# Performance work log

Hardware: AMD Instinct MI355X
Metric: run time of the kernel (lower is better)

## Reference

```python
import jax, jax.numpy as jnp
import numpy as np

N = 20000      # nodes
E = 400000     # directed edges
F_IN = 256     # node features
H, C = 16, 32  # heads, per-head channels (out_channels + beta_on, beta_on=0)
OUT = 32       # out_channels
HID = 128      # 4 * out_channels


def setup_inputs() -> dict:
    key = jax.random.key(0)
    ks = jax.random.split(key, 14)
    s = 0.05
    return {
        "x": jax.random.normal(ks[0], (N, F_IN), jnp.float32),
        "edge_index": jax.random.randint(ks[1], (2, E), 0, N, jnp.int32),
        "W1": jax.random.normal(ks[2], (F_IN, H * C), jnp.float32) * s,
        "att_src1": jax.random.normal(ks[3], (H, C), jnp.float32) * s,
        "att_dst1": jax.random.normal(ks[4], (H, C), jnp.float32) * s,
        "b1": jax.random.normal(ks[5], (C,), jnp.float32) * s,
        "W2": jax.random.normal(ks[6], (F_IN, H * C), jnp.float32) * s,
        "att_src2": jax.random.normal(ks[7], (H, C), jnp.float32) * s,
        "att_dst2": jax.random.normal(ks[8], (H, C), jnp.float32) * s,
        "b2": jax.random.normal(ks[9], (C,), jnp.float32) * s,
        "lin1_w": jax.random.normal(ks[10], (F_IN, HID), jnp.float32) * s,
        "lin1_b": jax.random.normal(ks[11], (HID,), jnp.float32) * s,
        "lin2_w": jax.random.normal(ks[12], (HID, OUT), jnp.float32) * s,
        "lin2_b": jax.random.normal(ks[13], (OUT,), jnp.float32) * s,
    }


def gat_conv(x, W, att_src, att_dst, bias, src, dst):
    """PyG GATConv: heads=H, concat=False (mean over heads), no self loops.
    src = message source node per edge, dst = aggregation (central) node."""
    h = (x @ W).reshape(-1, H, C)                 # [N, H, C]
    a_s = jnp.sum(h * att_src, axis=-1)           # [N, H]
    a_d = jnp.sum(h * att_dst, axis=-1)           # [N, H]
    alpha = jax.nn.leaky_relu(a_s[src] + a_d[dst], 0.2)  # [E, H]
    # numerically-stable segment softmax over edges grouped by dst
    m = jax.lax.stop_gradient(jax.ops.segment_max(alpha, dst, num_segments=N))
    m = jnp.where(jnp.isfinite(m), m, 0.0)        # empty segments -> -inf
    ex = jnp.exp(alpha - m[dst])                  # [E, H]
    den = jax.ops.segment_sum(ex, dst, num_segments=N)   # [N, H]
    coef = ex / (den[dst] + 1e-16)                # [E, H]
    msg = h[src] * coef[:, :, None]               # [E, H, C]
    out = jax.ops.segment_sum(msg, dst, num_segments=N)  # [N, H, C]
    return out.mean(axis=1) + bias                # concat=False -> head mean


def reference(x, edge_index, W1, att_src1, att_dst1, b1, W2, att_src2, att_dst2,
              b2, lin1_w, lin1_b, lin2_w, lin2_b):
    src = edge_index[0]
    dst = edge_index[1]
    # conv1: flow='source_to_target' -> aggregate at edge_index[1]
    x_in = jax.nn.elu(gat_conv(x, W1, att_src1, att_dst1, b1, src, dst))
    # conv2: flow='target_to_source' -> aggregate at edge_index[0]
    x_out = jax.nn.elu(gat_conv(x, W2, att_src2, att_dst2, b2, dst, src))
    x1 = jax.nn.elu(x @ lin1_w + lin1_b)
    x_self = jax.nn.elu(x1 @ lin2_w + lin2_b)
    return (x_in, x_out, x_self)
```

## Files before the change

### kernel.cpp

```cpp
#include <hip/hip_runtime.h>
#include <math.h>

#define NN 20000
#define EE 400000
#define FIN 256
#define HH 16
#define CC 32
#define HC 512
#define H8W 1024
#define HIDN 128
#define OUTC 32
#define WT 1024

typedef unsigned short u16;
typedef unsigned char u8;
typedef __attribute__((ext_vector_type(8))) short short8v;
typedef __attribute__((ext_vector_type(4))) float f32x4;
typedef __attribute__((ext_vector_type(2))) float f32x2;

__device__ inline u16 f2bf(float f) {
  unsigned u = __builtin_bit_cast(unsigned, f);
  unsigned r = (u + 0x7fffu + ((u >> 16) & 1u)) >> 16;
  return (u16)r;
}
__device__ inline float bf2f(u16 b) {
  unsigned u = ((unsigned)b) << 16;
  return __builtin_bit_cast(float, u);
}

__device__ __forceinline__ void gload16(const u16* g, u16* l) {
  __builtin_amdgcn_global_load_lds(
      (const __attribute__((address_space(1))) unsigned int*)g,
      (__attribute__((address_space(3))) unsigned int*)l, 16, 0, 0);
}

__device__ __forceinline__ void fp8x8_fma2(uint2 hv, float w, f32x2* acc) {
  f32x2 w2; w2.x = w; w2.y = w;
  f32x2 p0 = __builtin_amdgcn_cvt_pk_f32_fp8(hv.x, false);
  f32x2 p1 = __builtin_amdgcn_cvt_pk_f32_fp8(hv.x, true);
  f32x2 p2 = __builtin_amdgcn_cvt_pk_f32_fp8(hv.y, false);
  f32x2 p3 = __builtin_amdgcn_cvt_pk_f32_fp8(hv.y, true);
  acc[0] += p0 * w2;
  acc[1] += p1 * w2;
  acc[2] += p2 * w2;
  acc[3] += p3 * w2;
}

__global__ void k_prep_hist(const float* __restrict__ x, u16* __restrict__ xb,
                            const float* __restrict__ W1, const float* __restrict__ W2,
                            u16* __restrict__ wtc,
                            const float* __restrict__ L1, u16* __restrict__ lt1,
                            const float* __restrict__ L2, u16* __restrict__ lt2,
                            const int* __restrict__ ei, int* __restrict__ cur) {
  int b = blockIdx.x, t = threadIdx.x;
  if (b < 2500) {
    int i = b * 256 + t;
    float4 v0 = ((const float4*)x)[i * 2];
    float4 v1 = ((const float4*)x)[i * 2 + 1];
    short8v o;
    o[0] = (short)f2bf(v0.x); o[1] = (short)f2bf(v0.y);
    o[2] = (short)f2bf(v0.z); o[3] = (short)f2bf(v0.w);
    o[4] = (short)f2bf(v1.x); o[5] = (short)f2bf(v1.y);
    o[6] = (short)f2bf(v1.z); o[7] = (short)f2bf(v1.w);
    *(short8v*)(xb + (size_t)i * 8) = o;
  } else if (b < 3524) {
    int i = (b - 2500) * 256 + t;
    int n = i >> 8, k = i & 255;
    wtc[i] = f2bf(n < 512 ? W1[k * HC + n] : W2[k * HC + (n - 512)]);
  } else if (b < 3652) {
    int i = (b - 3524) * 256 + t;
    int n = i >> 8, k = i & 255;
    lt1[i] = f2bf(L1[k * HIDN + n]);
  } else if (b < 3668) {
    int i = (b - 3652) * 256 + t;
    int n = i >> 7, k = i & 127;
    lt2[i] = f2bf(L2[k * OUTC + n]);
  } else {
    int e = (b - 3668) * 256 + t;
    if (e < EE) {
      atomicAdd(&cur[ei[EE + e]], 1);
      atomicAdd(&cur[NN + ei[e]], 1);
    }
  }
}

__device__ void scan_one(int* cur, int* off, int* part) {
  const int t = threadIdx.x;
  const int CHK = 20;
  int base = t * CHK;
  int loc[CHK];
  int s = 0;
#pragma unroll
  for (int i = 0; i < CHK; ++i) {
    int idx = base + i;
    int v = (idx < NN) ? cur[idx] : 0;
    loc[i] = s;
    s += v;
  }
  part[t] = s;
  __syncthreads();
  for (int d = 1; d < 1024; d <<= 1) {
    int v2 = (t >= d) ? part[t - d] : 0;
    __syncthreads();
    part[t] += v2;
    __syncthreads();
  }
  int cbase = part[t] - s;
#pragma unroll
  for (int i = 0; i < CHK; ++i) {
    int idx = base + i;
    if (idx < NN) {
      int o = cbase + loc[i];
      off[idx] = o;
      cur[idx] = o;
    }
  }
  if (t == 1023) off[NN] = part[1023];
}

__global__ __launch_bounds__(1024) void k_scan(int* cur, int* off1, int* off2) {
  __shared__ int part[1024];
  if (blockIdx.x == 0) scan_one(cur, off1, part);
  else                 scan_one(cur + NN, off2, part);
}

__global__ void k_scatter(const int* __restrict__ ei, int* cur,
                          int* __restrict__ adj1, int* __restrict__ adj2) {
  int e = blockIdx.x * 256 + threadIdx.x;
  if (e < EE) {
    int s1 = ei[e], d1 = ei[EE + e];
    int p1 = atomicAdd(&cur[d1], 1);
    adj1[p1] = s1;
    int p2 = atomicAdd(&cur[NN + s1], 1);
    adj2[p2] = d1;
  }
}

__global__ __launch_bounds__(256) void k_gemm_big(const u16* __restrict__ A,
                                                  const u16* __restrict__ Bt,
                                                  const float* __restrict__ as1,
                                                  const float* __restrict__ ad1,
                                                  const float* __restrict__ as2,
                                                  const float* __restrict__ ad2,
                                                  u8* __restrict__ h8,
                                                  float* __restrict__ a_sA,
                                                  float* __restrict__ a_dA) {
  __shared__ u16 As[128 * 64];
  __shared__ u16 Bs[128 * 64];
  const int hw = blockIdx.x;
  const int logical = (hw & 7) * 157 + (hw >> 3);
  const int bm = (logical >> 3) * 128, bn = logical & 7;
  const int t = threadIdx.x;
  const int lane = t & 63, wave = t >> 6;
  const int wr = (wave >> 1) * 64, wc = (wave & 1) * 64;
  const int l15 = lane & 15, l4 = lane >> 4;
  const int rloc = lane >> 3;
  const int kc_src = (lane & 7) ^ rloc;
  const int K = FIN;

  f32x4 acc[4][4] = {};
  for (int k0 = 0; k0 < K; k0 += 64) {
    __syncthreads();
#pragma unroll
    for (int q = 0; q < 4; ++q) {
      const int rblk = q * 4 + wave;
      const int r = rblk * 8 + rloc;
      gload16(A + (size_t)(bm + r) * K + k0 + kc_src * 8, As + rblk * 512);
      gload16(Bt + (size_t)(bn * 128 + r) * K + k0 + kc_src * 8, Bs + rblk * 512);
    }
    __syncthreads();
#pragma unroll
    for (int kh = 0; kh < 2; ++kh) {
      const int kc = kh * 4 + l4;
      short8v af[4], bfr[4];
#pragma unroll
      for (int i = 0; i < 4; ++i) {
        int row = wr + i * 16 + l15;
        af[i] = *(const short8v*)(As + row * 64 + (kc ^ (row & 7)) * 8);
      }
#pragma unroll
      for (int j = 0; j < 4; ++j) {
        int row = wc + j * 16 + l15;
        bfr[j] = *(const short8v*)(Bs + row * 64 + (kc ^ (row & 7)) * 8);
      }
#pragma unroll
      for (int i = 0; i < 4; ++i)
#pragma unroll
        for (int j = 0; j < 4; ++j)
          acc[i][j] = __builtin_amdgcn_mfma_f32_16x16x32_bf16(af[i], bfr[j], acc[i][j], 0, 0, 0);
    }
  }

  const int conv = bn >> 2;
#pragma unroll
  for (int i = 0; i < 4; ++i)
#pragma unroll
    for (int j = 0; j < 4; ++j)
#pragma unroll
      for (int r = 0; r < 4; ++r) {
        int row = bm + wr + i * 16 + l4 * 4 + r;
        if (row >= NN) continue;
        int colb = bn * 128 + wc + j * 16 + l15;
        float v = acc[i][j][r];
        unsigned e8 = __builtin_amdgcn_cvt_pk_fp8_f32(v, v, 0, false);
        h8[(size_t)row * H8W + colb] = (u8)e8;
      }

  float asv[4], adv[4];
#pragma unroll
  for (int j = 0; j < 4; ++j) {
    int lc = (bn & 3) * 128 + wc + j * 16 + l15;
    int hh = lc >> 5, c = lc & 31;
    asv[j] = (conv ? as2 : as1)[hh * CC + c];
    adv[j] = (conv ? ad2 : ad1)[hh * CC + c];
  }
  const int hA = (bn & 3) * 4 + (wc >> 5);
  float* aS = a_sA + (size_t)conv * NN * HH;
  float* aD = a_dA + (size_t)conv * NN * HH;
#pragma unroll
  for (int i = 0; i < 4; ++i)
#pragma unroll
    for (int r = 0; r < 4; ++r) {
      float sAs = acc[i][0][r] * asv[0] + acc[i][1][r] * asv[1];
      float sAd = acc[i][0][r] * adv[0] + acc[i][1][r] * adv[1];
      float sBs = acc[i][2][r] * asv[2] + acc[i][3][r] * asv[3];
      float sBd = acc[i][2][r] * adv[2] + acc[i][3][r] * adv[3];
#pragma unroll
      for (int m = 1; m < 16; m <<= 1) {
        sAs += __shfl_xor(sAs, m);
        sAd += __shfl_xor(sAd, m);
        sBs += __shfl_xor(sBs, m);
        sBd += __shfl_xor(sBd, m);
      }
      int row = bm + wr + i * 16 + l4 * 4 + r;
      if (l15 == 0 && row < NN) {
        *(float2*)(aS + (size_t)row * HH + hA) = make_float2(sAs, sBs);
        *(float2*)(aD + (size_t)row * HH + hA) = make_float2(sAd, sBd);
      }
    }
}

__global__ __launch_bounds__(256) void k_self(const u16* __restrict__ A,
                                              const u16* __restrict__ lt1,
                                              const u16* __restrict__ lt2,
                                              const float* __restrict__ lin1_b,
                                              const float* __restrict__ lin2_b,
                                              float* __restrict__ outp) {
  __shared__ u16 smem[128 * 128];
  u16* As = smem;
  u16* Bs = smem + 128 * 64;
  const int t = threadIdx.x;
  const int lane = t & 63, wave = t >> 6;
  const int wr = (wave >> 1) * 64, wc = (wave & 1) * 64;
  const int bm = blockIdx.x * 128;
  const int l15 = lane & 15, l4 = lane >> 4;
  const int rloc = lane >> 3;
  const int kc_src = (lane & 7) ^ rloc;
  const int K = FIN;

  f32x4 acc[4][4] = {};
  for (int k0 = 0; k0 < K; k0 += 64) {
    __syncthreads();
#pragma unroll
    for (int q = 0; q < 4; ++q) {
      const int rblk = q * 4 + wave;
      const int r = rblk * 8 + rloc;
      gload16(A + (size_t)(bm + r) * K + k0 + kc_src * 8, As + rblk * 512);
      gload16(lt1 + (size_t)r * K + k0 + kc_src * 8, Bs + rblk * 512);
    }
    __syncthreads();
#pragma unroll
    for (int kh = 0; kh < 2; ++kh) {
      const int kc = kh * 4 + l4;
      short8v af[4], bfr[4];
#pragma unroll
      for (int i = 0; i < 4; ++i) {
        int row = wr + i * 16 + l15;
        af[i] = *(const short8v*)(As + row * 64 + (kc ^ (row & 7)) * 8);
      }
#pragma unroll
      for (int j = 0; j < 4; ++j) {
        int row = wc + j * 16 + l15;
        bfr[j] = *(const short8v*)(Bs + row * 64 + (kc ^ (row & 7)) * 8);
      }
#pragma unroll
      for (int i = 0; i < 4; ++i)
#pragma unroll
        for (int j = 0; j < 4; ++j)
          acc[i][j] = __builtin_amdgcn_mfma_f32_16x16x32_bf16(af[i], bfr[j], acc[i][j], 0, 0, 0);
    }
  }
  __syncthreads();
#pragma unroll
  for (int i = 0; i < 4; ++i)
#pragma unroll
    for (int j = 0; j < 4; ++j)
#pragma unroll
      for (int r = 0; r < 4; ++r) {
        int row = wr + i * 16 + l4 * 4 + r;
        int col = wc + j * 16 + l15;
        float v = acc[i][j][r] + lin1_b[col];
        v = v > 0.f ? v : (expf(v) - 1.f);
        smem[row * 128 + ((((col >> 3) ^ (row & 7))) << 3) + (col & 7)] = f2bf(v);
      }
  __syncthreads();
  f32x4 acc2[2][2] = {};
#pragma unroll
  for (int kk = 0; kk < 4; ++kk) {
    short8v af[2], bfr[2];
#pragma unroll
    for (int i = 0; i < 2; ++i) {
      int row2 = wave * 32 + i * 16 + l15;
      af[i] = *(const short8v*)(smem + row2 * 128 + (((kk * 4 + l4) ^ (row2 & 7)) << 3));
    }
#pragma unroll
    for (int j = 0; j < 2; ++j)
      bfr[j] = *(const short8v*)(lt2 + (size_t)(j * 16 + l15) * 128 + kk * 32 + l4 * 8);
#pragma unroll
    for (int i = 0; i < 2; ++i)
#pragma unroll
      for (int j = 0; j < 2; ++j)
        acc2[i][j] = __builtin_amdgcn_mfma_f32_16x16x32_bf16(af[i], bfr[j], acc2[i][j], 0, 0, 0);
  }
#pragma unroll
  for (int i = 0; i < 2; ++i)
#pragma unroll
    for (int j = 0; j < 2; ++j)
#pragma unroll
      for (int r = 0; r < 4; ++r) {
        int row = bm + wave * 32 + i * 16 + l4 * 4 + r;
        int col = j * 16 + l15;
        if (row < NN) {
          float v = acc2[i][j][r] + lin2_b[col];
          v = v > 0.f ? v : (expf(v) - 1.f);
          outp[(size_t)row * OUTC + col] = v;
        }
      }
}

__global__ __launch_bounds__(256) void k_edge(const int* __restrict__ adj1,
                                              const int* __restrict__ off1,
                                              const int* __restrict__ adj2,
                                              const int* __restrict__ off2,
                                              const float* __restrict__ a_sA,
                                              const float* __restrict__ a_dA,
                                              const u8* __restrict__ h8,
                                              const float* __restrict__ b1,
                                              const float* __restrict__ b2,
                                              float* __restrict__ out) {
  const int wv = threadIdx.x >> 6, lane = threadIdx.x & 63;
  const int gid = blockIdx.x * 4 + wv;
  const int conv = gid >= NN;
  const int node = gid - conv * NN;
  const int* __restrict__ adj = conv ? adj2 : adj1;
  const int* __restrict__ off = conv ? off2 : off1;
  const float* __restrict__ a_s = a_sA + (size_t)conv * NN * HH;
  const float* __restrict__ a_d = a_dA + (size_t)conv * NN * HH;
  const float* __restrict__ bias = conv ? b2 : b1;
  float* __restrict__ outp = out + (size_t)conv * NN * OUTC;
  const int e0 = off[node], e1 = off[node + 1];

  const int ea = lane >> 4, hh = lane & 15;
  const int h = lane >> 2, cg = lane & 3;
  const u8* hb = h8 + conv * HC + h * CC + cg * 8;
  const float adh = a_d[node * HH + hh];
  f32x2 acc0[4] = {}, acc1[4] = {};
  float den = 0.f;
  int p = e0;
  for (; p + 4 <= e1; p += 4) {
    int se = adj[p + ea];
    float al = a_s[se * HH + hh] + adh;
    al = al > 0.f ? al : 0.2f * al;
    float wgt = __expf(al);
    den += wgt;
    float w0 = __shfl(wgt, h);
    float w1 = __shfl(wgt, 16 + h);
    float w2 = __shfl(wgt, 32 + h);
    float w3 = __shfl(wgt, 48 + h);
    int s0 = adj[p], s1 = adj[p + 1], s2 = adj[p + 2], s3 = adj[p + 3];
    uint2 h0 = *(const uint2*)(hb + (size_t)s0 * H8W);
    uint2 h1 = *(const uint2*)(hb + (size_t)s1 * H8W);
    uint2 h2v = *(const uint2*)(hb + (size_t)s2 * H8W);
    uint2 h3 = *(const uint2*)(hb + (size_t)s3 * H8W);
    fp8x8_fma2(h0, w0, acc0);
    fp8x8_fma2(h1, w1, acc1);
    fp8x8_fma2(h2v, w2, acc0);
    fp8x8_fma2(h3, w3, acc1);
  }
  if (p < e1) {
    int pe = p + ea;
    float wgt = 0.f;
    if (pe < e1) {
      int se = adj[pe];
      float al = a_s[se * HH + hh] + adh;
      al = al > 0.f ? al : 0.2f * al;
      wgt = __expf(al);
    }
    den += wgt;
    float w0 = __shfl(wgt, h);
    float w1 = __shfl(wgt, 16 + h);
    float w2 = __shfl(wgt, 32 + h);
    {
      int s0 = adj[p];
      uint2 h0 = *(const uint2*)(hb + (size_t)s0 * H8W);
      fp8x8_fma2(h0, w0, acc0);
    }
    if (p + 1 < e1) {
      int s1 = adj[p + 1];
      uint2 h1 = *(const uint2*)(hb + (size_t)s1 * H8W);
      fp8x8_fma2(h1, w1, acc1);
    }
    if (p + 2 < e1) {
      int s2 = adj[p + 2];
      uint2 h2v = *(const uint2*)(hb + (size_t)s2 * H8W);
      fp8x8_fma2(h2v, w2, acc0);
    }
  }
  den += __shfl_xor(den, 16);
  den += __shfl_xor(den, 32);
  float inv = (1.f / 16.f) / (den + 1e-16f);
  const float ivh = __shfl(inv, h);
  float accf[8];
#pragma unroll
  for (int i = 0; i < 4; ++i) {
    f32x2 s2v = acc0[i] + acc1[i];
    accf[2 * i] = s2v.x * ivh;
    accf[2 * i + 1] = s2v.y * ivh;
  }
#pragma unroll
  for (int mk = 4; mk <= 32; mk <<= 1)
#pragma unroll
    for (int i = 0; i < 8; ++i) accf[i] += __shfl_xor(accf[i], mk);
  if (lane < 4) {
#pragma unroll
    for (int i = 0; i < 8; ++i) {
      int c = cg * 8 + i;
      float v = accf[i] + bias[c];
      v = v > 0.f ? v : (expf(v) - 1.f);
      outp[(size_t)node * OUTC + c] = v;
    }
  }
}

extern "C" void kernel_launch(void* const* d_in, const int* in_sizes, int n_in,
                              void* d_out, int out_size, void* d_ws, size_t ws_size,
                              hipStream_t stream) {
  const float* x = (const float*)d_in[0];
  const int* ei = (const int*)d_in[1];
  const float* W1 = (const float*)d_in[2];
  const float* att_src1 = (const float*)d_in[3];
  const float* att_dst1 = (const float*)d_in[4];
  const float* b1 = (const float*)d_in[5];
  const float* W2 = (const float*)d_in[6];
  const float* att_src2 = (const float*)d_in[7];
  const float* att_dst2 = (const float*)d_in[8];
  const float* b2 = (const float*)d_in[9];
  const float* lin1_w = (const float*)d_in[10];
  const float* lin1_b = (const float*)d_in[11];
  const float* lin2_w = (const float*)d_in[12];
  const float* lin2_b = (const float*)d_in[13];
  float* out = (float*)d_out;

  char* w = (char*)d_ws;
  u8* h8 = (u8*)w;          w += (size_t)NN * H8W;
  u16* x_bf = (u16*)w;      w += (size_t)NN * FIN * 2;
  u16* wtc = (u16*)w;       w += (size_t)WT * FIN * 2;
  u16* lt1 = (u16*)w;       w += (size_t)HIDN * FIN * 2;
  u16* lt2 = (u16*)w;       w += (size_t)OUTC * HIDN * 2;
  float* a_sA = (float*)w;  w += (size_t)2 * NN * HH * 4;
  float* a_dA = (float*)w;  w += (size_t)2 * NN * HH * 4;
  int* off1 = (int*)w;      w += (size_t)(NN + 1) * 4;
  int* off2 = (int*)w;      w += (size_t)(NN + 1) * 4;
  int* cur = (int*)w;       w += (size_t)2 * NN * 4;
  int* adj1 = (int*)w;      w += (size_t)EE * 4;
  int* adj2 = (int*)w;      w += (size_t)EE * 4;

  const int EB = (EE + 255) / 256;

  hipMemsetAsync(cur, 0, (size_t)2 * NN * 4, stream);
  k_prep_hist<<<3668 + EB, 256, 0, stream>>>(x, x_bf, W1, W2, wtc, lin1_w, lt1,
                                             lin2_w, lt2, ei, cur);
  k_scan<<<2, 1024, 0, stream>>>(cur, off1, off2);
  k_scatter<<<EB, 256, 0, stream>>>(ei, cur, adj1, adj2);

  k_gemm_big<<<1256, 256, 0, stream>>>(x_bf, wtc, att_src1, att_dst1,
                                       att_src2, att_dst2, h8, a_sA, a_dA);
  k_self<<<157, 256, 0, stream>>>(x_bf, lt1, lt2, lin1_b, lin2_b,
                                  out + (size_t)2 * NN * OUTC);

  k_edge<<<2 * (NN / 4), 256, 0, stream>>>(adj1, off1, adj2, off2, a_sA, a_dA,
                                           h8, b1, b2, out);
}
```

Measured before the change: 238.9 us.

## Merge CSR build into cooperative kernel and fuse self-MLP into GAT GEMM

Replaces the memset, histogram/prep, two-block scan and scatter kernels with one persistent cooperative kernel that uses grid-wide syncs between phases, and parallelises the scan across 158 blocks. It also folds the self-MLP GEMM into the big GAT GEMM launch as extra blocks. The intent is to cut launch gaps and the serial single-block scan. In exchange, grid.sync barriers add cost, and the cooperative grid of 1024 blocks must be co-resident.

```diff
diff --git a/kernel.cpp b/kernel.cpp
--- a/kernel.cpp
+++ b/kernel.cpp
@@ -1,5 +1,8 @@
 #include <hip/hip_runtime.h>
+#include <hip/hip_cooperative_groups.h>
 #include <math.h>
+
+namespace cg = cooperative_groups;
 
 #define NN 20000
 #define EE 400000
@@ -11,6 +14,7 @@
 #define HIDN 128
 #define OUTC 32
 #define WT 1024
+#define GRID_B 1024
 
 typedef unsigned short u16;
 typedef unsigned char u8;
@@ -22,10 +26,6 @@
   unsigned u = __builtin_bit_cast(unsigned, f);
   unsigned r = (u + 0x7fffu + ((u >> 16) & 1u)) >> 16;
   return (u16)r;
-}
-__device__ inline float bf2f(u16 b) {
-  unsigned u = ((unsigned)b) << 16;
-  return __builtin_bit_cast(float, u);
 }
 
 __device__ __forceinline__ void gload16(const u16* g, u16* l) {
@@ -46,15 +46,23 @@
   acc[3] += p3 * w2;
 }
 
-__global__ void k_prep_hist(const float* __restrict__ x, u16* __restrict__ xb,
-                            const float* __restrict__ W1, const float* __restrict__ W2,
-                            u16* __restrict__ wtc,
-                            const float* __restrict__ L1, u16* __restrict__ lt1,
-                            const float* __restrict__ L2, u16* __restrict__ lt2,
-                            const int* __restrict__ ei, int* __restrict__ cur) {
-  int b = blockIdx.x, t = threadIdx.x;
-  if (b < 2500) {
-    int i = b * 256 + t;
+__global__ __launch_bounds__(256, 4) void k_build(
+    const float* __restrict__ x, u16* __restrict__ xb,
+    const float* __restrict__ W1, const float* __restrict__ W2, u16* __restrict__ wtc,
+    const float* __restrict__ L1, u16* __restrict__ lt1,
+    const float* __restrict__ L2, u16* __restrict__ lt2,
+    const int* __restrict__ ei, int* __restrict__ cur,
+    int* __restrict__ off1, int* __restrict__ off2,
+    int* __restrict__ adj1, int* __restrict__ adj2, int* __restrict__ bsum) {
+  cg::grid_group grid = cg::this_grid();
+  const int tx = threadIdx.x;
+  const int tid = blockIdx.x * 256 + tx;
+  const int NTH = GRID_B * 256;
+
+  for (int i = tid; i < 2 * NN; i += NTH) cur[i] = 0;
+  grid.sync();
+
+  for (int i = tid; i < NN * FIN / 8; i += NTH) {
     float4 v0 = ((const float4*)x)[i * 2];
     float4 v1 = ((const float4*)x)[i * 2 + 1];
     short8v o;
@@ -63,71 +71,69 @@
     o[4] = (short)f2bf(v1.x); o[5] = (short)f2bf(v1.y);
     o[6] = (short)f2bf(v1.z); o[7] = (short)f2bf(v1.w);
     *(short8v*)(xb + (size_t)i * 8) = o;
-  } else if (b < 3524) {
-    int i = (b - 2500) * 256 + t;
+  }
+  for (int i = tid; i < WT * FIN; i += NTH) {
     int n = i >> 8, k = i & 255;
     wtc[i] = f2bf(n < 512 ? W1[k * HC + n] : W2[k * HC + (n - 512)]);
-  } else if (b < 3652) {
-    int i = (b - 3524) * 256 + t;
-    int n = i >> 8, k = i & 255;
-    lt1[i] = f2bf(L1[k * HIDN + n]);
-  } else if (b < 3668) {
-    int i = (b - 3652) * 256 + t;
-    int n = i >> 7, k = i & 127;
-    lt2[i] = f2bf(L2[k * OUTC + n]);
-  } else {
-    int e = (b - 3668) * 256 + t;
-    if (e < EE) {
-      atomicAdd(&cur[ei[EE + e]], 1);
-      atomicAdd(&cur[NN + ei[e]], 1);
-    }
-  }
-}
-
-__device__ void scan_one(int* cur, int* off, int* part) {
-  const int t = threadIdx.x;
-  const int CHK = 20;
-  int base = t * CHK;
-  int loc[CHK];
-  int s = 0;
-#pragma unroll
-  for (int i = 0; i < CHK; ++i) {
-    int idx = base + i;
-    int v = (idx < NN) ? cur[idx] : 0;
-    loc[i] = s;
-    s += v;
-  }
-  part[t] = s;
-  __syncthreads();
-  for (int d = 1; d < 1024; d <<= 1) {
-    int v2 = (t >= d) ? part[t - d] : 0;
+  }
+  if (tid < HIDN * FIN) {
+    int n = tid >> 8, k = tid & 255;
+    lt1[tid] = f2bf(L1[k * HIDN + n]);
+  }
+  if (tid < OUTC * HIDN) {
+    int n = tid >> 7, k = tid & 127;
+    lt2[tid] = f2bf(L2[k * OUTC + n]);
+  }
+  for (int e = tid; e < EE; e += NTH) {
+    atomicAdd(&cur[ei[EE + e]], 1);
+    atomicAdd(&cur[NN + ei[e]], 1);
+  }
+  grid.sync();
+
+  __shared__ int sd[256];
+  int v = 0, incl = 0, cv = 0, idx0 = 0;
+  if (blockIdx.x < 158) {
+    cv = blockIdx.x / 79;
+    idx0 = (blockIdx.x % 79) * 256 + tx;
+    v = (idx0 < NN) ? cur[cv * NN + idx0] : 0;
+    sd[tx] = v;
     __syncthreads();
-    part[t] += v2;
+    for (int d = 1; d < 256; d <<= 1) {
+      int t2 = (tx >= d) ? sd[tx - d] : 0;
+      __syncthreads();
+      sd[tx] += t2;
+      __syncthreads();
+    }
+    incl = sd[tx];
+    if (tx == 255) bsum[blockIdx.x] = incl;
+  }
+  grid.sync();
+  if (blockIdx.x == 0) {
+    int val = (tx < 158) ? bsum[tx] : 0;
+    sd[tx] = val;
     __syncthreads();
-  }
-  int cbase = part[t] - s;
-#pragma unroll
-  for (int i = 0; i < CHK; ++i) {
-    int idx = base + i;
-    if (idx < NN) {
-      int o = cbase + loc[i];
-      off[idx] = o;
-      cur[idx] = o;
-    }
-  }
-  if (t == 1023) off[NN] = part[1023];
-}
-
-__global__ __launch_bounds__(1024) void k_scan(int* cur, int* off1, int* off2) {
-  __shared__ int part[1024];
-  if (blockIdx.x == 0) scan_one(cur, off1, part);
-  else                 scan_one(cur + NN, off2, part);
-}
-
-__global__ void k_scatter(const int* __restrict__ ei, int* cur,
-                          int* __restrict__ adj1, int* __restrict__ adj2) {
-  int e = blockIdx.x * 256 + threadIdx.x;
-  if (e < EE) {
+    for (int d = 1; d < 256; d <<= 1) {
+      int t2 = (tx >= d && (tx - d) / 79 == tx / 79) ? sd[tx - d] : 0;
+      __syncthreads();
+      sd[tx] += t2;
+      __syncthreads();
+    }
+    if (tx < 158) bsum[tx] = sd[tx] - val;
+  }
+  grid.sync();
+  if (blockIdx.x < 158) {
+    int base = bsum[blockIdx.x];
+    int excl = base + incl - v;
+    int* off = cv ? off2 : off1;
+    if (idx0 < NN) {
+      off[idx0] = excl;
+      cur[cv * NN + idx0] = excl;
+    }
+    if (idx0 == 0) off[NN] = EE;
+  }
+  grid.sync();
+
+  for (int e = tid; e < EE; e += NTH) {
     int s1 = ei[e], d1 = ei[EE + e];
     int p1 = atomicAdd(&cur[d1], 1);
     adj1[p1] = s1;
@@ -136,20 +142,17 @@
   }
 }
 
-__global__ __launch_bounds__(256) void k_gemm_big(const u16* __restrict__ A,
-                                                  const u16* __restrict__ Bt,
-                                                  const float* __restrict__ as1,
-                                                  const float* __restrict__ ad1,
-                                                  const float* __restrict__ as2,
-                                                  const float* __restrict__ ad2,
-                                                  u8* __restrict__ h8,
-                                                  float* __restrict__ a_sA,
-                                                  float* __restrict__ a_dA) {
-  __shared__ u16 As[128 * 64];
-  __shared__ u16 Bs[128 * 64];
-  const int hw = blockIdx.x;
-  const int logical = (hw & 7) * 157 + (hw >> 3);
-  const int bm = (logical >> 3) * 128, bn = logical & 7;
+__global__ __launch_bounds__(256) void k_gemmself(
+    const u16* __restrict__ A, const u16* __restrict__ Bt,
+    const float* __restrict__ as1, const float* __restrict__ ad1,
+    const float* __restrict__ as2, const float* __restrict__ ad2,
+    u8* __restrict__ h8, float* __restrict__ a_sA, float* __restrict__ a_dA,
+    const u16* __restrict__ lt1, const u16* __restrict__ lt2,
+    const float* __restrict__ lin1_b, const float* __restrict__ lin2_b,
+    float* __restrict__ out3) {
+  __shared__ u16 smem[128 * 128];
+  u16* As = smem;
+  u16* Bs = smem + 128 * 64;
   const int t = threadIdx.x;
   const int lane = t & 63, wave = t >> 6;
   const int wr = (wave >> 1) * 64, wc = (wave & 1) * 64;
@@ -158,184 +161,172 @@
   const int kc_src = (lane & 7) ^ rloc;
   const int K = FIN;
 
-  f32x4 acc[4][4] = {};
-  for (int k0 = 0; k0 < K; k0 += 64) {
+  if (blockIdx.x < 1256) {
+    const int hw = blockIdx.x;
+    const int logical = (hw & 7) * 157 + (hw >> 3);
+    const int bm = (logical >> 3) * 128, bn = logical & 7;
+
+    f32x4 acc[4][4] = {};
+    for (int k0 = 0; k0 < K; k0 += 64) {
+      __syncthreads();
+#pragma unroll
+      for (int q = 0; q < 4; ++q) {
+        const int rblk = q * 4 + wave;
+        const int r = rblk * 8 + rloc;
+        gload16(A + (size_t)(bm + r) * K + k0 + kc_src * 8, As + rblk * 512);
+        gload16(Bt + (size_t)(bn * 128 + r) * K + k0 + kc_src * 8, Bs + rblk * 512);
+      }
+      __syncthreads();
+#pragma unroll
+      for (int kh = 0; kh < 2; ++kh) {
+        const int kc = kh * 4 + l4;
+        short8v af[4], bfr[4];
+#pragma unroll
+        for (int i = 0; i < 4; ++i) {
+          int row = wr + i * 16 + l15;
+          af[i] = *(const short8v*)(As + row * 64 + (kc ^ (row & 7)) * 8);
+        }
+#pragma unroll
+        for (int j = 0; j < 4; ++j) {
+          int row = wc + j * 16 + l15;
+          bfr[j] = *(const short8v*)(Bs + row * 64 + (kc ^ (row & 7)) * 8);
+        }
+#pragma unroll
+        for (int i = 0; i < 4; ++i)
+#pragma unroll
+          for (int j = 0; j < 4; ++j)
+            acc[i][j] = __builtin_amdgcn_mfma_f32_16x16x32_bf16(af[i], bfr[j], acc[i][j], 0, 0, 0);
+      }
+    }
+
+    const int conv = bn >> 2;
+#pragma unroll
+    for (int i = 0; i < 4; ++i)
+#pragma unroll
+      for (int j = 0; j < 4; ++j)
+#pragma unroll
+        for (int r = 0; r < 4; ++r) {
+          int row = bm + wr + i * 16 + l4 * 4 + r;
+          if (row >= NN) continue;
+          int colb = bn * 128 + wc + j * 16 + l15;
+          float v = acc[i][j][r];
+          unsigned e8 = __builtin_amdgcn_cvt_pk_fp8_f32(v, v, 0, false);
+          h8[(size_t)row * H8W + colb] = (u8)e8;
+        }
+
+    float asv[4], adv[4];
+#pragma unroll
+    for (int j = 0; j < 4; ++j) {
+      int lc = (bn & 3) * 128 + wc + j * 16 + l15;
+      int hh = lc >> 5, c = lc & 31;
+      asv[j] = (conv ? as2 : as1)[hh * CC + c];
+      adv[j] = (conv ? ad2 : ad1)[hh * CC + c];
+    }
+    const int hA = (bn & 3) * 4 + (wc >> 5);
+    float* aS = a_sA + (size_t)conv * NN * HH;
+    float* aD = a_dA + (size_t)conv * NN * HH;
+#pragma unroll
+    for (int i = 0; i < 4; ++i)
+#pragma unroll
+      for (int r = 0; r < 4; ++r) {
+        float sAs = acc[i][0][r] * asv[0] + acc[i][1][r] * asv[1];
+        float sAd = acc[i][0][r] * adv[0] + acc[i][1][r] * adv[1];
+        float sBs = acc[i][2][r] * asv[2] + acc[i][3][r] * asv[3];
+        float sBd = acc[i][2][r] * adv[2] + acc[i][3][r] * adv[3];
+#pragma unroll
+        for (int m = 1; m < 16; m <<= 1) {
+          sAs += __shfl_xor(sAs, m);
+          sAd += __shfl_xor(sAd, m);
+          sBs += __shfl_xor(sBs, m);
+          sBd += __shfl_xor(sBd, m);
+        }
+        int row = bm + wr + i * 16 + l4 * 4 + r;
+        if (l15 == 0 && row < NN) {
+          *(float2*)(aS + (size_t)row * HH + hA) = make_float2(sAs, sBs);
+          *(float2*)(aD + (size_t)row * HH + hA) = make_float2(sAd, sBd);
+        }
+      }
+  } else {
+    const int bm = (blockIdx.x - 1256) * 128;
+    f32x4 acc[4][4] = {};
+    for (int k0 = 0; k0 < K; k0 += 64) {
+      __syncthreads();
+#pragma unroll
+      for (int q = 0; q < 4; ++q) {
+        const int rblk = q * 4 + wave;
+        const int r = rblk * 8 + rloc;
+        gload16(A + (size_t)(bm + r) * K + k0 + kc_src * 8, As + rblk * 512);
+        gload16(lt1 + (size_t)r * K + k0 + kc_src * 8, Bs + rblk * 512);
+      }
+      __syncthreads();
+#pragma unroll
+      for (int kh = 0; kh < 2; ++kh) {
+        const int kc = kh * 4 + l4;
+        short8v af[4], bfr[4];
+#pragma unroll
+        for (int i = 0; i < 4; ++i) {
+          int row = wr + i * 16 + l15;
+          af[i] = *(const short8v*)(As + row * 64 + (kc ^ (row & 7)) * 8);
+        }
+#pragma unroll
+        for (int j = 0; j < 4; ++j) {
+          int row = wc + j * 16 + l15;
+          bfr[j] = *(const short8v*)(Bs + row * 64 + (kc ^ (row & 7)) * 8);
+        }
+#pragma unroll
+        for (int i = 0; i < 4; ++i)
+#pragma unroll
+          for (int j = 0; j < 4; ++j)
+            acc[i][j] = __builtin_amdgcn_mfma_f32_16x16x32_bf16(af[i], bfr[j], acc[i][j], 0, 0, 0);
+      }
+    }
     __syncthreads();
 #pragma unroll
-    for (int q = 0; q < 4; ++q) {
-      const int rblk = q * 4 + wave;
-      const int r = rblk * 8 + rloc;
-      gload16(A + (size_t)(bm + r) * K + k0 + kc_src * 8, As + rblk * 512);
-      gload16(Bt + (size_t)(bn * 128 + r) * K + k0 + kc_src * 8, Bs + rblk * 512);
-    }
+    for (int i = 0; i < 4; ++i)
+#pragma unroll
+      for (int j = 0; j < 4; ++j)
+#pragma unroll
+        for (int r = 0; r < 4; ++r) {
+          int row = wr + i * 16 + l4 * 4 + r;
+          int col = wc + j * 16 + l15;
+          float v = acc[i][j][r] + lin1_b[col];
+          v = v > 0.f ? v : (expf(v) - 1.f);
+          smem[row * 128 + ((((col >> 3) ^ (row & 7))) << 3) + (col & 7)] = f2bf(v);
+        }
     __syncthreads();
-#pragma unroll
-    for (int kh = 0; kh < 2; ++kh) {
-      const int kc = kh * 4 + l4;
-      short8v af[4], bfr[4];
-#pragma unroll
-      for (int i = 0; i < 4; ++i) {
-        int row = wr + i * 16 + l15;
-        af[i] = *(const short8v*)(As + row * 64 + (kc ^ (row & 7)) * 8);
-      }
-#pragma unroll
-      for (int j = 0; j < 4; ++j) {
-        int row = wc + j * 16 + l15;
-        bfr[j] = *(const short8v*)(Bs + row * 64 + (kc ^ (row & 7)) * 8);
-      }
-#pragma unroll
-      for (int i = 0; i < 4; ++i)
-#pragma unroll
-        for (int j = 0; j < 4; ++j)
-          acc[i][j] = __builtin_amdgcn_mfma_f32_16x16x32_bf16(af[i], bfr[j], acc[i][j], 0, 0, 0);
-    }
-  }
-
-  const int conv = bn >> 2;
-#pragma unroll
-  for (int i = 0; i < 4; ++i)
-#pragma unroll
-    for (int j = 0; j < 4; ++j)
-#pragma unroll
-      for (int r = 0; r < 4; ++r) {
-        int row = bm + wr + i * 16 + l4 * 4 + r;
-        if (row >= NN) continue;
-        int colb = bn * 128 + wc + j * 16 + l15;
-        float v = acc[i][j][r];
-        unsigned e8 = __builtin_amdgcn_cvt_pk_fp8_f32(v, v, 0, false);
-        h8[(size_t)row * H8W + colb] = (u8)e8;
-      }
-
-  float asv[4], adv[4];
-#pragma unroll
-  for (int j = 0; j < 4; ++j) {
-    int lc = (bn & 3) * 128 + wc + j * 16 + l15;
-    int hh = lc >> 5, c = lc & 31;
-    asv[j] = (conv ? as2 : as1)[hh * CC + c];
-    adv[j] = (conv ? ad2 : ad1)[hh * CC + c];
-  }
-  const int hA = (bn & 3) * 4 + (wc >> 5);
-  float* aS = a_sA + (size_t)conv * NN * HH;
-  float* aD = a_dA + (size_t)conv * NN * HH;
-#pragma unroll
-  for (int i = 0; i < 4; ++i)
-#pragma unroll
-    for (int r = 0; r < 4; ++r) {
-      float sAs = acc[i][0][r] * asv[0] + acc[i][1][r] * asv[1];
-      float sAd = acc[i][0][r] * adv[0] + acc[i][1][r] * adv[1];
-      float sBs = acc[i][2][r] * asv[2] + acc[i][3][r] * asv[3];
-      float sBd = acc[i][2][r] * adv[2] + acc[i][3][r] * adv[3];
-#pragma unroll
-      for (int m = 1; m < 16; m <<= 1) {
-        sAs += __shfl_xor(sAs, m);
-        sAd += __shfl_xor(sAd, m);
-        sBs += __shfl_xor(sBs, m);
-        sBd += __shfl_xor(sBd, m);
-      }
-      int row = bm + wr + i * 16 + l4 * 4 + r;
-      if (l15 == 0 && row < NN) {
-        *(float2*)(aS + (size_t)row * HH + hA) = make_float2(sAs, sBs);
-        *(float2*)(aD + (size_t)row * HH + hA) = make_float2(sAd, sBd);
-      }
-    }
-}
-
-__global__ __launch_bounds__(256) void k_self(const u16* __restrict__ A,
-                                              const u16* __restrict__ lt1,
-                                              const u16* __restrict__ lt2,
-                                              const float* __restrict__ lin1_b,
-                                              const float* __restrict__ lin2_b,
-                                              float* __restrict__ outp) {
-  __shared__ u16 smem[128 * 128];
-  u16* As = smem;
-  u16* Bs = smem + 128 * 64;
-  const int t = threadIdx.x;
-  const int lane = t & 63, wave = t >> 6;
-  const int wr = (wave >> 1) * 64, wc = (wave & 1) * 64;
-  const int bm = blockIdx.x * 128;
-  const int l15 = lane & 15, l4 = lane >> 4;
-  const int rloc = lane >> 3;
-  const int kc_src = (lane & 7) ^ rloc;
-  const int K = FIN;
-
-  f32x4 acc[4][4] = {};
-  for (int k0 = 0; k0 < K; k0 += 64) {
-    __syncthreads();
-#pragma unroll
-    for (int q = 0; q < 4; ++q) {
-      const int rblk = q * 4 + wave;
-      const int r = rblk * 8 + rloc;
-      gload16(A + (size_t)(bm + r) * K + k0 + kc_src * 8, As + rblk * 512);
-      gload16(lt1 + (size_t)r * K + k0 + kc_src * 8, Bs + rblk * 512);
-    }
-    __syncthreads();
-#pragma unroll
-    for (int kh = 0; kh < 2; ++kh) {
-      const int kc = kh * 4 + l4;
-      short8v af[4], bfr[4];
-#pragma unroll
-      for (int i = 0; i < 4; ++i) {
-        int row = wr + i * 16 + l15;
-        af[i] = *(const short8v*)(As + row * 64 + (kc ^ (row & 7)) * 8);
-      }
-#pragma unroll
-      for (int j = 0; j < 4; ++j) {
-        int row = wc + j * 16 + l15;
-        bfr[j] = *(const short8v*)(Bs + row * 64 + (kc ^ (row & 7)) * 8);
-      }
-#pragma unroll
-      for (int i = 0; i < 4; ++i)
-#pragma unroll
-        for (int j = 0; j < 4; ++j)
-          acc[i][j] = __builtin_amdgcn_mfma_f32_16x16x32_bf16(af[i], bfr[j], acc[i][j], 0, 0, 0);
-    }
-  }
-  __syncthreads();
-#pragma unroll
-  for (int i = 0; i < 4; ++i)
-#pragma unroll
-    for (int j = 0; j < 4; ++j)
-#pragma unroll
-      for (int r = 0; r < 4; ++r) {
-        int row = wr + i * 16 + l4 * 4 + r;
-        int col = wc + j * 16 + l15;
-        float v = acc[i][j][r] + lin1_b[col];
-        v = v > 0.f ? v : (expf(v) - 1.f);
-        smem[row * 128 + ((((col >> 3) ^ (row & 7))) << 3) + (col & 7)] = f2bf(v);
-      }
-  __syncthreads();
-  f32x4 acc2[2][2] = {};
-#pragma unroll
-  for (int kk = 0; kk < 4; ++kk) {
-    short8v af[2], bfr[2];
-#pragma unroll
-    for (int i = 0; i < 2; ++i) {
-      int row2 = wave * 32 + i * 16 + l15;
-      af[i] = *(const short8v*)(smem + row2 * 128 + (((kk * 4 + l4) ^ (row2 & 7)) << 3));
-    }
-#pragma unroll
-    for (int j = 0; j < 2; ++j)
-      bfr[j] = *(const short8v*)(lt2 + (size_t)(j * 16 + l15) * 128 + kk * 32 + l4 * 8);
+    f32x4 acc2[2][2] = {};
+#pragma unroll
+    for (int kk = 0; kk < 4; ++kk) {
+      short8v af[2], bfr[2];
+#pragma unroll
+      for (int i = 0; i < 2; ++i) {
+        int row2 = wave * 32 + i * 16 + l15;
+        af[i] = *(const short8v*)(smem + row2 * 128 + (((kk * 4 + l4) ^ (row2 & 7)) << 3));
+      }
+#pragma unroll
+      for (int j = 0; j < 2; ++j)
+        bfr[j] = *(const short8v*)(lt2 + (size_t)(j * 16 + l15) * 128 + kk * 32 + l4 * 8);
+#pragma unroll
+      for (int i = 0; i < 2; ++i)
+#pragma unroll
+        for (int j = 0; j < 2; ++j)
+          acc2[i][j] = __builtin_amdgcn_mfma_f32_16x16x32_bf16(af[i], bfr[j], acc2[i][j], 0, 0, 0);
+    }
 #pragma unroll
     for (int i = 0; i < 2; ++i)
 #pragma unroll
       for (int j = 0; j < 2; ++j)
-        acc2[i][j] = __builtin_amdgcn_mfma_f32_16x16x32_bf16(af[i], bfr[j], acc2[i][j], 0, 0, 0);
-  }
-#pragma unroll
-  for (int i = 0; i < 2; ++i)
-#pragma unroll
-    for (int j = 0; j < 2; ++j)
-#pragma unroll
-      for (int r = 0; r < 4; ++r) {
-        int row = bm + wave * 32 + i * 16 + l4 * 4 + r;
-        int col = j * 16 + l15;
-        if (row < NN) {
-          float v = acc2[i][j][r] + lin2_b[col];
-          v = v > 0.f ? v : (expf(v) - 1.f);
-          outp[(size_t)row * OUTC + col] = v;
-        }
-      }
+#pragma unroll
+        for (int r = 0; r < 4; ++r) {
+          int row = bm + wave * 32 + i * 16 + l4 * 4 + r;
+          int col = j * 16 + l15;
+          if (row < NN) {
+            float v = acc2[i][j][r] + lin2_b[col];
+            v = v > 0.f ? v : (expf(v) - 1.f);
+            out3[(size_t)row * OUTC + col] = v;
+          }
+        }
+  }
 }
 
 __global__ __launch_bounds__(256) void k_edge(const int* __restrict__ adj1,
@@ -474,19 +465,18 @@
   int* cur = (int*)w;       w += (size_t)2 * NN * 4;
   int* adj1 = (int*)w;      w += (size_t)EE * 4;
   int* adj2 = (int*)w;      w += (size_t)EE * 4;
-
-  const int EB = (EE + 255) / 256;
-
-  hipMemsetAsync(cur, 0, (size_t)2 * NN * 4, stream);
-  k_prep_hist<<<3668 + EB, 256, 0, stream>>>(x, x_bf, W1, W2, wtc, lin1_w, lt1,
-                                             lin2_w, lt2, ei, cur);
-  k_scan<<<2, 1024, 0, stream>>>(cur, off1, off2);
-  k_scatter<<<EB, 256, 0, stream>>>(ei, cur, adj1, adj2);
-
-  k_gemm_big<<<1256, 256, 0, stream>>>(x_bf, wtc, att_src1, att_dst1,
-                                       att_src2, att_dst2, h8, a_sA, a_dA);
-  k_self<<<157, 256, 0, stream>>>(x_bf, lt1, lt2, lin1_b, lin2_b,
-                                  out + (size_t)2 * NN * OUTC);
+  int* bsum = (int*)w;      w += (size_t)256 * 4;
+
+  void* args[] = {(void*)&x, (void*)&x_bf, (void*)&W1, (void*)&W2, (void*)&wtc,
+                  (void*)&lin1_w, (void*)&lt1, (void*)&lin2_w, (void*)&lt2,
+                  (void*)&ei, (void*)&cur, (void*)&off1, (void*)&off2,
+                  (void*)&adj1, (void*)&adj2, (void*)&bsum};
+  hipLaunchCooperativeKernel((void*)k_build, dim3(GRID_B), dim3(256), args, 0, stream);
+
+  float* out3 = out + (size_t)2 * NN * OUTC;
+  k_gemmself<<<1256 + 157, 256, 0, stream>>>(x_bf, wtc, att_src1, att_dst1,
+                                             att_src2, att_dst2, h8, a_sA, a_dA,
+                                             lt1, lt2, lin1_b, lin2_b, out3);
 
   k_edge<<<2 * (NN / 4), 256, 0, stream>>>(adj1, off1, adj2, off2, a_sA, a_dA,
                                            h8, b1, b2, out);
```

Result: slower. 679.6 us (+184.5%).
